# Optimization experiments

Measured on AMD Instinct MI355X. Metric: run time of the kernel, lower is better.

The kernel has to match this reference:

```python
import jax, jax.numpy as jnp
import numpy as np

B = 32          # decode batch (num sequences)
H = 32          # query heads
HKV = 8         # kv heads (GQA group = H // HKV = 4)
DH = 128        # head dim
MAX_LIVE = 2048 # compact cache budget per sequence (max_live_count)
S = B * MAX_LIVE  # total compact slots
SCALE = DH ** -0.5


def setup_inputs() -> dict:
    key = jax.random.key(0)
    ks = jax.random.split(key, 6)
    q = jax.random.normal(ks[0], (B, H, DH), dtype=jnp.float32)
    k = jax.random.normal(ks[1], (B, HKV, DH), dtype=jnp.float32)
    v = jax.random.normal(ks[2], (B, HKV, DH), dtype=jnp.float32)
    compact_k_cache = jax.random.normal(ks[3], (S, HKV, DH), dtype=jnp.float32)
    compact_v_cache = jax.random.normal(ks[4], (S, HKV, DH), dtype=jnp.float32)
    base_offsets = (jnp.arange(B, dtype=jnp.int32) * MAX_LIVE)
    live_counts = jax.random.randint(ks[5], (B,), 1, MAX_LIVE + 1).astype(jnp.int32)
    # new token is stored at the last live slot of each sequence
    slot_mapping = base_offsets + live_counts - 1
    return {
        "q": q, "k": k, "v": v,
        "compact_k_cache": compact_k_cache,
        "compact_v_cache": compact_v_cache,
        "base_offsets": base_offsets,
        "live_counts": live_counts,
        "slot_mapping": slot_mapping,
    }


def reference(q, k, v, compact_k_cache, compact_v_cache,
              base_offsets, live_counts, slot_mapping):
    # ---- store_compact_kvcache: scatter new token k/v into compact caches ----
    valid = slot_mapping >= 0                       # slot == -1 -> skip
    safe_slot = jnp.where(valid, slot_mapping, 0)
    m = valid[:, None, None]
    kc = compact_k_cache.at[safe_slot].set(
        jnp.where(m, k, compact_k_cache[safe_slot]))
    vc = compact_v_cache.at[safe_slot].set(
        jnp.where(m, v, compact_v_cache[safe_slot]))

    # ---- compact_decode_attention over [base_offset, base_offset+live_count) ----
    pos = jnp.arange(MAX_LIVE, dtype=jnp.int32)            # [L]
    mask = pos[None, :] < live_counts[:, None]             # [B, L]
    idx = base_offsets[:, None] + pos[None, :]             # [B, L]
    safe_idx = jnp.where(mask, idx, 0)
    kg = kc[safe_idx]                                      # [B, L, HKV, DH]
    vg = vc[safe_idx]                                      # [B, L, HKV, DH]

    G = H // HKV
    qg = q.reshape(B, HKV, G, DH)                          # group query heads by kv head
    scores = jnp.einsum('bhgd,blhd->bhgl', qg, kg) * SCALE # [B, HKV, G, L]
    scores = jnp.where(mask[:, None, None, :], scores, jnp.finfo(scores.dtype).min)
    p = jax.nn.softmax(scores, axis=-1)
    o = jnp.einsum('bhgl,blhd->bhgd', p, vg).reshape(B, H, DH)
    return o
```

## Files before the change

### kernel.cpp

```cpp
#include <hip/hip_runtime.h>
#include <math.h>

#define NB 32
#define NH 32
#define NKV 8
#define NG 4
#define DH 128
#define MAXL 2048
#define CHUNK 128
#define NCH (MAXL / CHUNK)
#define ROWF (NKV * DH)

#define SCALE_LOG2E 0.12752966529379885f

template <int CTRL>
__device__ __forceinline__ float dpp_add(float x) {
    int y = __builtin_amdgcn_update_dpp(0, __float_as_int(x), CTRL, 0xf, 0xf, false);
    return x + __int_as_float(y);
}
__device__ __forceinline__ float half_reduce_sum(float d) {
    d = dpp_add<0x111>(d);
    d = dpp_add<0x112>(d);
    d = dpp_add<0x114>(d);
    d = dpp_add<0x118>(d);
    d = dpp_add<0x142>(d);
    return d;
}

__global__ __launch_bounds__(256) void attn_partial_kernel(
    const float* __restrict__ q,
    const float* __restrict__ knew,
    const float* __restrict__ vnew,
    const float* __restrict__ kcache,
    const float* __restrict__ vcache,
    const int* __restrict__ base_offsets,
    const int* __restrict__ live_counts,
    const int* __restrict__ slot_mapping,
    float* __restrict__ pml,
    float* __restrict__ pacc)
{
    const int c = blockIdx.x;
    const int h = blockIdx.y;
    const int b = blockIdx.z;

    const int live = live_counts[b];
    const int p0 = c * CHUNK;
    if (p0 >= live) return;

    const int base = base_offsets[b];
    const int rep  = slot_mapping[b] - base;

    const int tid  = (int)threadIdx.x;
    const int wave = tid >> 6;
    const int lane = tid & 63;
    const int half = lane >> 5;
    const int ql   = lane & 31;

    __shared__ float  sc[NG][CHUNK];
    __shared__ float4 sacc[NG][8][32];

    float4 qv[NG];
#pragma unroll
    for (int g = 0; g < NG; ++g)
        qv[g] = *(const float4*)(q + (size_t)(b * NH + h * NG + g) * DH + ql * 4);

    const float4 kn4 = *(const float4*)(knew + (size_t)(b * NKV + h) * DH + ql * 4);
    const float4 vn4 = *(const float4*)(vnew + (size_t)(b * NKV + h) * DH + ql * 4);

    const int lim = live - 1;
    const int pw0 = p0 + wave * 32;
    const float* kb = kcache + (size_t)base * ROWF + h * DH + ql * 4;
    const float* vb = vcache + (size_t)base * ROWF + h * DH + ql * 4;

#pragma unroll
    for (int i = 0; i < 16; ++i) {
        const int p  = pw0 + 2 * i + half;
        const int pc = min(p, lim);
        float4 kk = *(const float4*)(kb + ((size_t)pc << 10));
        if (pc == rep) kk = kn4;
#pragma unroll
        for (int g = 0; g < NG; ++g) {
            float d = kk.x * qv[g].x + kk.y * qv[g].y +
                      kk.z * qv[g].z + kk.w * qv[g].w;
            d = half_reduce_sum(d);
            const float s = (p <= lim) ? d * SCALE_LOG2E : -INFINITY;
            if (ql == 31) sc[g][p - p0] = s;
        }
    }
    __syncthreads();

    {
        const int g = wave;
        const float s0 = sc[g][lane];
        const float s1 = sc[g][64 + lane];
        float m = fmaxf(s0, s1);
#pragma unroll
        for (int off = 1; off < 64; off <<= 1)
            m = fmaxf(m, __shfl_xor(m, off));
        const float e0 = exp2f(s0 - m);
        const float e1 = exp2f(s1 - m);
        float l = e0 + e1;
#pragma unroll
        for (int off = 1; off < 64; off <<= 1)
            l += __shfl_xor(l, off);
        sc[g][lane]      = e0;
        sc[g][64 + lane] = e1;
        if (lane == 0) {
            const size_t pidx = ((size_t)(b * NKV + h) * NG + g) * NCH + c;
            pml[pidx * 2]     = m;
            pml[pidx * 2 + 1] = l;
        }
    }
    __syncthreads();

    float4 acc[NG];
#pragma unroll
    for (int g = 0; g < NG; ++g) acc[g] = make_float4(0.f, 0.f, 0.f, 0.f);

#pragma unroll
    for (int i = 0; i < 16; ++i) {
        const int p  = pw0 + 2 * i + half;
        const int pc = min(p, lim);
        float4 vv = *(const float4*)(vb + ((size_t)pc << 10));
        if (pc == rep) vv = vn4;
        const int pos = p - p0;
#pragma unroll
        for (int g = 0; g < NG; ++g) {
            const float w = sc[g][pos];
            acc[g].x += w * vv.x;
            acc[g].y += w * vv.y;
            acc[g].z += w * vv.z;
            acc[g].w += w * vv.w;
        }
    }

    const int hw = wave * 2 + half;
#pragma unroll
    for (int g = 0; g < NG; ++g)
        sacc[g][hw][ql] = acc[g];
    __syncthreads();

    if (half == 0) {
        const int g = wave;
        float4 o = make_float4(0.f, 0.f, 0.f, 0.f);
#pragma unroll
        for (int j = 0; j < 8; ++j) {
            const float4 a = sacc[g][j][ql];
            o.x += a.x; o.y += a.y; o.z += a.z; o.w += a.w;
        }
        const size_t pidx = ((size_t)(b * NKV + h) * NG + g) * NCH + c;
        *(float4*)(pacc + pidx * DH + ql * 4) = o;
    }
}

__global__ __launch_bounds__(256) void attn_combine_kernel(
    const int* __restrict__ live_counts,
    const float* __restrict__ pml,
    const float* __restrict__ pacc,
    float* __restrict__ out)
{
    const int h = blockIdx.x;
    const int b = blockIdx.y;
    const int g = (int)threadIdx.x >> 6;
    const int lane = (int)threadIdx.x & 63;

    const int live = live_counts[b];
    const int nc = (live + CHUNK - 1) / CHUNK;
    const size_t pbase = ((size_t)(b * NKV + h) * NG + g) * NCH;

    float M = -INFINITY;
    for (int cj = 0; cj < nc; ++cj)
        M = fmaxf(M, pml[(pbase + cj) * 2]);
    float L = 0.f;
    for (int cj = 0; cj < nc; ++cj)
        L += exp2f(pml[(pbase + cj) * 2] - M) * pml[(pbase + cj) * 2 + 1];
    float2 o = make_float2(0.f, 0.f);
    for (int cj = 0; cj < nc; ++cj) {
        const float w = exp2f(pml[(pbase + cj) * 2] - M);
        const float2 a = *(const float2*)(pacc + (pbase + cj) * DH + lane * 2);
        o.x += w * a.x;
        o.y += w * a.y;
    }
    const float inv = 1.f / L;
    o.x *= inv; o.y *= inv;
    *(float2*)(out + (size_t)(b * NH + h * NG + g) * DH + lane * 2) = o;
}

extern "C" void kernel_launch(void* const* d_in, const int* in_sizes, int n_in,
                              void* d_out, int out_size, void* d_ws, size_t ws_size,
                              hipStream_t stream) {
    const float* q    = (const float*)d_in[0];
    const float* knew = (const float*)d_in[1];
    const float* vnew = (const float*)d_in[2];
    const float* kc   = (const float*)d_in[3];
    const float* vc   = (const float*)d_in[4];
    const int* base   = (const int*)d_in[5];
    const int* live   = (const int*)d_in[6];
    const int* slot   = (const int*)d_in[7];
    float* out = (float*)d_out;

    float* pml  = (float*)d_ws;
    float* pacc = pml + (size_t)2 * NB * NKV * NG * NCH;

    dim3 grid1(NCH, NKV, NB);
    attn_partial_kernel<<<grid1, 256, 0, stream>>>(q, knew, vnew, kc, vc,
                                                   base, live, slot, pml, pacc);
    dim3 grid2(NKV, NB);
    attn_combine_kernel<<<grid2, 256, 0, stream>>>(live, pml, pacc, out);
}
```

Baseline: 489.6 us.

## Cover all KV heads per block so each slot row is read contiguously

The partial kernel now has each block handle one 32-position chunk for all 8 KV heads. Each half-wave owns one head, so a full 4KB cache row is read by the 256 threads in one contiguous access instead of per-head 512B strips. Because each half-wave now covers the whole chunk for its head, the cross-wave shared-memory reduction of accumulators and its barrier are gone. In exchange there are four times as many chunks, so the combine kernel has more partial results to merge, the workspace grows, and each thread runs a longer serial loop over positions.

```diff
diff --git a/kernel.cpp b/kernel.cpp
--- a/kernel.cpp
+++ b/kernel.cpp
@@ -7,7 +7,7 @@
 #define NG 4
 #define DH 128
 #define MAXL 2048
-#define CHUNK 128
+#define CHUNK 32
 #define NCH (MAXL / CHUNK)
 #define ROWF (NKV * DH)
 
@@ -40,8 +40,7 @@
     float* __restrict__ pacc)
 {
     const int c = blockIdx.x;
-    const int h = blockIdx.y;
-    const int b = blockIdx.z;
+    const int b = blockIdx.y;
 
     const int live = live_counts[b];
     const int p0 = c * CHUNK;
@@ -51,30 +50,27 @@
     const int rep  = slot_mapping[b] - base;
 
     const int tid  = (int)threadIdx.x;
-    const int wave = tid >> 6;
     const int lane = tid & 63;
-    const int half = lane >> 5;
     const int ql   = lane & 31;
+    const int hw   = tid >> 5;
 
-    __shared__ float  sc[NG][CHUNK];
-    __shared__ float4 sacc[NG][8][32];
+    __shared__ float sc[NKV][NG][CHUNK];
 
     float4 qv[NG];
 #pragma unroll
     for (int g = 0; g < NG; ++g)
-        qv[g] = *(const float4*)(q + (size_t)(b * NH + h * NG + g) * DH + ql * 4);
+        qv[g] = *(const float4*)(q + (size_t)(b * NH + hw * NG + g) * DH + ql * 4);
 
-    const float4 kn4 = *(const float4*)(knew + (size_t)(b * NKV + h) * DH + ql * 4);
-    const float4 vn4 = *(const float4*)(vnew + (size_t)(b * NKV + h) * DH + ql * 4);
+    const float4 kn4 = *(const float4*)(knew + (size_t)(b * NKV + hw) * DH + ql * 4);
+    const float4 vn4 = *(const float4*)(vnew + (size_t)(b * NKV + hw) * DH + ql * 4);
 
     const int lim = live - 1;
-    const int pw0 = p0 + wave * 32;
-    const float* kb = kcache + (size_t)base * ROWF + h * DH + ql * 4;
-    const float* vb = vcache + (size_t)base * ROWF + h * DH + ql * 4;
+    const float* kb = kcache + (size_t)base * ROWF + tid * 4;
+    const float* vb = vcache + (size_t)base * ROWF + tid * 4;
 
-#pragma unroll
-    for (int i = 0; i < 16; ++i) {
-        const int p  = pw0 + 2 * i + half;
+#pragma unroll 8
+    for (int i = 0; i < CHUNK; ++i) {
+        const int p  = p0 + i;
         const int pc = min(p, lim);
         float4 kk = *(const float4*)(kb + ((size_t)pc << 10));
         if (pc == rep) kk = kn4;
@@ -84,29 +80,26 @@
                       kk.z * qv[g].z + kk.w * qv[g].w;
             d = half_reduce_sum(d);
             const float s = (p <= lim) ? d * SCALE_LOG2E : -INFINITY;
-            if (ql == 31) sc[g][p - p0] = s;
+            if (ql == 31) sc[hw][g][i] = s;
         }
     }
     __syncthreads();
 
-    {
-        const int g = wave;
-        const float s0 = sc[g][lane];
-        const float s1 = sc[g][64 + lane];
-        float m = fmaxf(s0, s1);
 #pragma unroll
-        for (int off = 1; off < 64; off <<= 1)
+    for (int g = 0; g < NG; ++g) {
+        const float s = sc[hw][g][ql];
+        float m = s;
+#pragma unroll
+        for (int off = 1; off < 32; off <<= 1)
             m = fmaxf(m, __shfl_xor(m, off));
-        const float e0 = exp2f(s0 - m);
-        const float e1 = exp2f(s1 - m);
-        float l = e0 + e1;
+        const float e = exp2f(s - m);
+        float l = e;
 #pragma unroll
-        for (int off = 1; off < 64; off <<= 1)
+        for (int off = 1; off < 32; off <<= 1)
             l += __shfl_xor(l, off);
-        sc[g][lane]      = e0;
-        sc[g][64 + lane] = e1;
-        if (lane == 0) {
-            const size_t pidx = ((size_t)(b * NKV + h) * NG + g) * NCH + c;
+        sc[hw][g][ql] = e;
+        if (ql == 0) {
+            const size_t pidx = ((size_t)(b * NKV + hw) * NG + g) * NCH + c;
             pml[pidx * 2]     = m;
             pml[pidx * 2 + 1] = l;
         }
@@ -117,16 +110,15 @@
 #pragma unroll
     for (int g = 0; g < NG; ++g) acc[g] = make_float4(0.f, 0.f, 0.f, 0.f);
 
-#pragma unroll
-    for (int i = 0; i < 16; ++i) {
-        const int p  = pw0 + 2 * i + half;
+#pragma unroll 8
+    for (int i = 0; i < CHUNK; ++i) {
+        const int p  = p0 + i;
         const int pc = min(p, lim);
         float4 vv = *(const float4*)(vb + ((size_t)pc << 10));
         if (pc == rep) vv = vn4;
-        const int pos = p - p0;
 #pragma unroll
         for (int g = 0; g < NG; ++g) {
-            const float w = sc[g][pos];
+            const float w = sc[hw][g][i];
             acc[g].x += w * vv.x;
             acc[g].y += w * vv.y;
             acc[g].z += w * vv.z;
@@ -134,22 +126,10 @@
         }
     }
 
-    const int hw = wave * 2 + half;
 #pragma unroll
-    for (int g = 0; g < NG; ++g)
-        sacc[g][hw][ql] = acc[g];
-    __syncthreads();
-
-    if (half == 0) {
-        const int g = wave;
-        float4 o = make_float4(0.f, 0.f, 0.f, 0.f);
-#pragma unroll
-        for (int j = 0; j < 8; ++j) {
-            const float4 a = sacc[g][j][ql];
-            o.x += a.x; o.y += a.y; o.z += a.z; o.w += a.w;
-        }
-        const size_t pidx = ((size_t)(b * NKV + h) * NG + g) * NCH + c;
-        *(float4*)(pacc + pidx * DH + ql * 4) = o;
+    for (int g = 0; g < NG; ++g) {
+        const size_t pidx = ((size_t)(b * NKV + hw) * NG + g) * NCH + c;
+        *(float4*)(pacc + pidx * DH + ql * 4) = acc[g];
     }
 }
 
@@ -202,7 +182,7 @@
     float* pml  = (float*)d_ws;
     float* pacc = pml + (size_t)2 * NB * NKV * NG * NCH;
 
-    dim3 grid1(NCH, NKV, NB);
+    dim3 grid1(NCH, NB);
     attn_partial_kernel<<<grid1, 256, 0, stream>>>(q, knew, vnew, kc, vc,
                                                    base, live, slot, pml, pacc);
     dim3 grid2(NKV, NB);
```

After: 502.3 us. 2.6% more time.
